# Kernel tuning notes

Hardware: AMD Instinct MI355X
Metric: run time of the kernel (lower is better)

The kernel has to match this reference:

```python
import jax, jax.numpy as jnp
import numpy as np

B, S, D_MODEL, H, NLAYERS, NHEADS = 16, 512, 768, 640, 2, 10
D_ATT = 2 * H  # 1280
HEAD_DIM = D_ATT // NHEADS  # 128


def _lstm_dir(xp, Whh, lengths, reverse):
    # xp: [B,S,4H] precomputed input projection (+bias); packed-sequence semantics:
    # state frozen and output zeroed for t >= length. torch gate order: i,f,g,o.
    Bs, Ss, H4 = xp.shape
    Hh = H4 // 4
    xpT = jnp.swapaxes(xp, 0, 1)  # [S,B,4H]
    ts = jnp.arange(Ss)
    if reverse:
        xpT = xpT[::-1]
        ts = ts[::-1]

    def step(carry, inp):
        h, c = carry
        x_t, t = inp
        g = x_t + h @ Whh.T
        i, f, gg, o = jnp.split(g, 4, axis=-1)
        i = jax.nn.sigmoid(i)
        f = jax.nn.sigmoid(f)
        gg = jnp.tanh(gg)
        o = jax.nn.sigmoid(o)
        c2 = f * c + i * gg
        h2 = o * jnp.tanh(c2)
        valid = (t < lengths)[:, None]
        h = jnp.where(valid, h2, h)
        c = jnp.where(valid, c2, c)
        return (h, c), jnp.where(valid, h, jnp.zeros_like(h))

    init = (jnp.zeros((Bs, Hh), xp.dtype), jnp.zeros((Bs, Hh), xp.dtype))
    _, ys = jax.lax.scan(step, init, (xpT, ts))
    if reverse:
        ys = ys[::-1]
    return jnp.swapaxes(ys, 0, 1)  # [B,S,H]


def _bilstm_layer(x, Wih, Whh, b, lengths):
    # Wih: [2,4H,in], Whh: [2,4H,H], b: [2,4H] (b_ih+b_hh combined)
    outs = []
    for d, rev in ((0, False), (1, True)):
        xp = jnp.einsum('bsi,gi->bsg', x, Wih[d]) + b[d]
        outs.append(_lstm_dir(xp, Whh[d], lengths, rev))
    return jnp.concatenate(outs, axis=-1)  # [B,S,2H]


def _forward(c_a_embeds, c_mask, c_lengths, Wih0, Whh0, b0, Wih1, Whh1, b1,
             Wq, bq, Wk, bk, Wv, bv):
    h = _bilstm_layer(c_a_embeds, Wih0, Whh0, b0, c_lengths)
    h = _bilstm_layer(h, Wih1, Whh1, b1, c_lengths)
    Bb, Ss, Dd = h.shape
    q = (h @ Wq.T + bq).reshape(Bb, Ss, NHEADS, HEAD_DIM)
    k = (h @ Wk.T + bk).reshape(Bb, Ss, NHEADS, HEAD_DIM)
    v = (h @ Wv.T + bv).reshape(Bb, Ss, NHEADS, HEAD_DIM)
    scores = jnp.einsum('bqhd,bkhd->bhqk', q, k) / np.float32(np.sqrt(HEAD_DIM))
    scores = scores + c_mask  # additive HF-style mask [B,1,1,S]
    probs = jax.nn.softmax(scores, axis=-1)
    ctx = jnp.einsum('bhqk,bkhd->bqhd', probs, v).reshape(Bb, Ss, Dd)
    return h + ctx


def setup_inputs() -> dict:
    key = jax.random.key(0)
    ks = jax.random.split(key, 20)
    c_a_embeds = jax.random.normal(ks[0], (B, S, D_MODEL), dtype=jnp.float32)
    c_lengths = jax.random.randint(ks[1], (B,), S // 2, S + 1, dtype=jnp.int32)
    valid = jnp.arange(S)[None, :] < c_lengths[:, None]
    c_mask = jnp.where(valid, 0.0, -10000.0).astype(jnp.float32)[:, None, None, :]
    sc = 1.0 / np.sqrt(H)

    def u(k, shape):
        return jax.random.uniform(k, shape, jnp.float32, -sc, sc)

    Wih0 = u(ks[2], (2, 4 * H, D_MODEL))
    Whh0 = u(ks[3], (2, 4 * H, H))
    b0 = u(ks[4], (2, 4 * H))
    Wih1 = u(ks[5], (2, 4 * H, 2 * H))
    Whh1 = u(ks[6], (2, 4 * H, H))
    b1 = u(ks[7], (2, 4 * H))
    sa = 1.0 / np.sqrt(D_ATT)
    Wq = jax.random.uniform(ks[8], (D_ATT, D_ATT), jnp.float32, -sa, sa)
    bq = jnp.zeros((D_ATT,), jnp.float32)
    Wk = jax.random.uniform(ks[9], (D_ATT, D_ATT), jnp.float32, -sa, sa)
    bk = jnp.zeros((D_ATT,), jnp.float32)
    Wv = jax.random.uniform(ks[10], (D_ATT, D_ATT), jnp.float32, -sa, sa)
    bv = jnp.zeros((D_ATT,), jnp.float32)
    return dict(c_a_embeds=c_a_embeds, c_mask=c_mask, c_lengths=c_lengths,
                Wih0=Wih0, Whh0=Whh0, b0=b0, Wih1=Wih1, Whh1=Whh1, b1=b1,
                Wq=Wq, bq=bq, Wk=Wk, bk=bk, Wv=Wv, bv=bv)


def reference(c_a_embeds, c_mask, c_lengths, Wih0, Whh0, b0, Wih1, Whh1, b1,
              Wq, bq, Wk, bk, Wv, bv):
    return _forward(c_a_embeds, c_mask, c_lengths, Wih0, Whh0, b0,
                    Wih1, Whh1, b1, Wq, bq, Wk, bk, Wv, bv)
```

## Files before the change

kernel.cpp:

```cpp
#include <hip/hip_runtime.h>

typedef __attribute__((ext_vector_type(8))) short short8;
typedef __attribute__((ext_vector_type(4))) float f32x4;
typedef __attribute__((ext_vector_type(4))) unsigned int u32x4;

#define MFMA(a,b,c) __builtin_amdgcn_mfma_f32_16x16x32_bf16((a),(b),(c),0,0,0)

#define B_  16
#define S_  512
#define DM_ 768
#define H_  640
#define G4_ 2560
#define DA_ 1280
#define NH_ 10
#define HD_ 128

static __device__ __forceinline__ unsigned short f2bf(float v) {
  unsigned u = __builtin_bit_cast(unsigned, v);
  u = (u + 0x7fffu + ((u >> 16) & 1u)) >> 16;
  return (unsigned short)u;
}
static __device__ __forceinline__ float bf2f(unsigned short u) {
  return __builtin_bit_cast(float, (unsigned)u << 16);
}
static __device__ __forceinline__ float sigm(float x) { return 1.0f / (1.0f + __expf(-x)); }
static __device__ __forceinline__ float tanh_c(float x) {
  x = fminf(fmaxf(x, -15.0f), 15.0f);
  float e = __expf(2.0f * x);
  return (e - 1.0f) / (e + 1.0f);
}

static __device__ __forceinline__ u32x4 load_coh16(const void* p) {
  u32x4 r;
  asm volatile("global_load_dwordx4 %0, %1, off sc0 sc1"
               : "=v"(r) : "v"(p) : "memory");
  return r;
}
static __device__ __forceinline__ void store_coh_u16(void* p, unsigned v) {
  asm volatile("global_store_short %0, %1, off sc0 sc1"
               :: "v"(p), "v"(v) : "memory");
}
static __device__ __forceinline__ void store_coh_u32(void* p, unsigned v) {
  asm volatile("global_store_dword %0, %1, off sc0 sc1"
               :: "v"(p), "v"(v) : "memory");
}
static __device__ __forceinline__ unsigned load_coh_u32(const void* p) {
  unsigned r;
  asm volatile("global_load_dword %0, %1, off sc0 sc1"
               : "=v"(r) : "v"(p) : "memory");
  return r;
}
#define WAIT_VM0() asm volatile("s_waitcnt vmcnt(0)" ::: "memory")

__global__ __launch_bounds__(256)
void cast_f32_bf16(const float* __restrict__ src, unsigned short* __restrict__ dst, int n4) {
  int i = blockIdx.x * 256 + threadIdx.x;
  if (i >= n4) return;
  float4 v = reinterpret_cast<const float4*>(src)[i];
  ushort4 o;
  o.x = f2bf(v.x); o.y = f2bf(v.y); o.z = f2bf(v.z); o.w = f2bf(v.w);
  reinterpret_cast<ushort4*>(dst)[i] = o;
}

__device__ __forceinline__ void gload_lds16(void* lds, const void* g) {
  __builtin_amdgcn_global_load_lds(
      (const __attribute__((address_space(1))) unsigned int*)g,
      (__attribute__((address_space(3))) unsigned int*)lds, 16, 0, 0);
}

template<int OUT_MODE>
__global__ __launch_bounds__(256)
void gemm_abt(const unsigned short* __restrict__ A, const unsigned short* __restrict__ W,
              const float* __restrict__ bias, void* __restrict__ Cout,
              int M, int N, int K) {
  __shared__ unsigned short lA[128 * 32];
  __shared__ unsigned short lB[128 * 32];
  const int tid = threadIdx.x;
  const int lane = tid & 63, wid = tid >> 6;
  const int nbn = N >> 7;
  const int mi = blockIdx.x / nbn, ni = blockIdx.x % nbn;
  const int l15 = lane & 15, lq = lane >> 4;

  f32x4 acc[4][4] = {};

  for (int k0 = 0; k0 < K; k0 += 32) {
#pragma unroll
    for (int part = 0; part < 2; ++part) {
      int linear = part * 256 + tid;
      int r = linear >> 2, cc = linear & 3;
      const unsigned short* ga = A + (size_t)(mi * 128 + r) * K + k0 + cc * 8;
      const unsigned short* gb = W + (size_t)(ni * 128 + r) * K + k0 + cc * 8;
      gload_lds16(&lA[(part * 256 + wid * 64) * 8], ga);
      gload_lds16(&lB[(part * 256 + wid * 64) * 8], gb);
    }
    __syncthreads();
    const int wm = (wid >> 1) * 64, wn = (wid & 1) * 64;
    short8 af[4], bfr[4];
#pragma unroll
    for (int m = 0; m < 4; ++m)
      af[m] = *(const short8*)&lA[(wm + m * 16 + l15) * 32 + lq * 8];
#pragma unroll
    for (int n = 0; n < 4; ++n)
      bfr[n] = *(const short8*)&lB[(wn + n * 16 + l15) * 32 + lq * 8];
#pragma unroll
    for (int m = 0; m < 4; ++m)
#pragma unroll
      for (int n = 0; n < 4; ++n)
        acc[m][n] = MFMA(af[m], bfr[n], acc[m][n]);
    __syncthreads();
  }

  const int wm = (wid >> 1) * 64, wn = (wid & 1) * 64;
#pragma unroll
  for (int n = 0; n < 4; ++n) {
    int col = ni * 128 + wn + n * 16 + l15;
    float bv = bias[col];
#pragma unroll
    for (int m = 0; m < 4; ++m) {
#pragma unroll
      for (int r = 0; r < 4; ++r) {
        int row = mi * 128 + wm + m * 16 + lq * 4 + r;
        float v = acc[m][n][r] + bv;
        if (OUT_MODE == 1) {
          ((unsigned short*)Cout)[(size_t)row * N + col] = f2bf(v);
        } else if (OUT_MODE == 2) {
          int bb = row >> 9, s = row & 511, hh = col >> 7, d = col & 127;
          ((unsigned short*)Cout)[(((size_t)(bb * NH_ + hh) * HD_ + d) << 9) + s] = f2bf(v);
        } else {
          int gate = col / 640, unit = col % 640;
          int slice = unit / 20, uu = unit % 20;
          int bb = row >> 9, tt = row & 511;
          size_t idx = (((size_t)slice * S_ + tt) * B_ + bb) * 80 + gate * 20 + uu;
          if (OUT_MODE == 3) ((float*)Cout)[idx] = v;
          else               ((unsigned short*)Cout)[idx] = f2bf(v);
        }
      }
    }
  }
}

template<bool XPF32>
__global__ __launch_bounds__(320)
void bilstm_layer(const void* __restrict__ xp_,
                  const unsigned short* __restrict__ whh_g,
                  const int* __restrict__ lengths,
                  unsigned short* __restrict__ h_ex,
                  int* __restrict__ flags, int flag_base,
                  unsigned short* __restrict__ out_bf)
{
  __shared__ unsigned short whh[80 * 648];
  __shared__ unsigned short hbuf[16 * 648];
  __shared__ float pre[16 * 80];
  __shared__ float xpbuf[16 * 80];
  __shared__ int len_s[16];

  const int tid = threadIdx.x;
  const int lane = tid & 63, wid = tid >> 6;
  const int wg = blockIdx.x;
  const int dir = wg >> 5, slice = wg & 31;
  const int J0 = slice * 20;
  const int l15 = lane & 15, lq = lane >> 4;

  for (int c = tid; c < 80 * 160; c += 320) {
    int r = c / 160, c4 = c % 160;
    int grow = (r / 20) * H_ + J0 + (r % 20);
    *(ushort4*)&whh[r * 648 + c4 * 4] =
        *(const ushort4*)&whh_g[((size_t)dir * G4_ + grow) * H_ + c4 * 4];
  }
  if (tid < 16) len_s[tid] = lengths[tid];
  __syncthreads();

  const int gb = tid / 20, gu = tid % 20;
  float c_st = 0.f, h_st = 0.f;

  const char* xps;
  if (XPF32)
    xps = (const char*)xp_ + ((size_t)dir * 32 + slice) * S_ * B_ * 80 * 4;
  else
    xps = (const char*)xp_ + ((size_t)dir * 32 + slice) * S_ * B_ * 80 * 2;

  float4  xv_f;
  ushort4 xv_h;
  {
    int t0 = dir ? (S_ - 1) : 0;
    if (XPF32) xv_f = *(const float4*)(xps + ((size_t)t0 * 1280 + tid * 4) * 4);
    else       xv_h = *(const ushort4*)(xps + ((size_t)t0 * 1280 + tid * 4) * 2);
  }

  for (int s = 0; s < S_; ++s) {
    const int t = dir ? (S_ - 1 - s) : s;
    float4  xn_f;
    ushort4 xn_h;
    {
      int tn = dir ? (S_ - 2 - s) : (s + 1);
      tn = tn < 0 ? 0 : (tn > S_ - 1 ? S_ - 1 : tn);
      if (XPF32) xn_f = *(const float4*)(xps + ((size_t)tn * 1280 + tid * 4) * 4);
      else       xn_h = *(const ushort4*)(xps + ((size_t)tn * 1280 + tid * 4) * 2);
    }

    {
      const unsigned short* src = h_ex + (size_t)(dir * 2 + (s & 1)) * B_ * H_;
      u32x4 hv[4];
      int bs[4], os[4];
#pragma unroll
      for (int j = 0; j < 4; ++j) {
        int c = tid + j * 320;
        bs[j] = c / 80; os[j] = c % 80;
        hv[j] = load_coh16(src + (size_t)bs[j] * 640 + os[j] * 8);
      }
      WAIT_VM0();
      __builtin_amdgcn_sched_barrier(0);
#pragma unroll
      for (int j = 0; j < 4; ++j)
        *(u32x4*)&hbuf[bs[j] * 648 + os[j] * 8] = hv[j];
    }
    if (XPF32) {
      *(float4*)&xpbuf[tid * 4] = xv_f;
    } else {
      *(ushort4*)&((unsigned short*)xpbuf)[tid * 4] = xv_h;
    }
    __syncthreads();

    f32x4 acc0 = {0.f, 0.f, 0.f, 0.f}, acc1 = {0.f, 0.f, 0.f, 0.f};
#pragma unroll
    for (int kk = 0; kk < 20; kk += 2) {
      short8 a0 = *(const short8*)&hbuf[l15 * 648 + kk * 32 + lq * 8];
      short8 b0v = *(const short8*)&whh[(wid * 16 + l15) * 648 + kk * 32 + lq * 8];
      acc0 = MFMA(a0, b0v, acc0);
      short8 a1 = *(const short8*)&hbuf[l15 * 648 + (kk + 1) * 32 + lq * 8];
      short8 b1v = *(const short8*)&whh[(wid * 16 + l15) * 648 + (kk + 1) * 32 + lq * 8];
      acc1 = MFMA(a1, b1v, acc1);
    }
#pragma unroll
    for (int r = 0; r < 4; ++r)
      pre[(lq * 4 + r) * 80 + wid * 16 + l15] = acc0[r] + acc1[r];
    __syncthreads();

    {
      float xi, xf, xg, xo;
      if (XPF32) {
        xi = xpbuf[gb * 80 + gu];
        xf = xpbuf[gb * 80 + 20 + gu];
        xg = xpbuf[gb * 80 + 40 + gu];
        xo = xpbuf[gb * 80 + 60 + gu];
      } else {
        const unsigned short* xb = (const unsigned short*)xpbuf;
        xi = bf2f(xb[gb * 80 + gu]);
        xf = bf2f(xb[gb * 80 + 20 + gu]);
        xg = bf2f(xb[gb * 80 + 40 + gu]);
        xo = bf2f(xb[gb * 80 + 60 + gu]);
      }
      float gi = pre[gb * 80 + gu]      + xi;
      float gf = pre[gb * 80 + 20 + gu] + xf;
      float gg = pre[gb * 80 + 40 + gu] + xg;
      float go = pre[gb * 80 + 60 + gu] + xo;
      float i_ = sigm(gi), f_ = sigm(gf);
      float g_ = tanh_c(gg), o_ = sigm(go);
      float c2 = f_ * c_st + i_ * g_;
      float h2 = o_ * tanh_c(c2);
      bool valid = t < len_s[gb];
      c_st = valid ? c2 : c_st;
      h_st = valid ? h2 : h_st;
      unsigned hb = f2bf(h_st);
      store_coh_u16(h_ex + (size_t)(dir * 2 + ((s + 1) & 1)) * B_ * H_
                         + (size_t)gb * H_ + J0 + gu, hb);
      float yv = valid ? h_st : 0.f;
      out_bf[((size_t)(gb * S_ + t)) * DA_ + dir * H_ + J0 + gu] = f2bf(yv);
    }

    WAIT_VM0();
    __syncthreads();
    const int target = flag_base + s + 1;
    if (tid == 0)
      store_coh_u32(flags + (size_t)wg * 32, (unsigned)target);
    if (wid == 0) {
      const int* fp = flags + (size_t)(dir * 32 + (lane & 31)) * 32;
      for (;;) {
        unsigned v = load_coh_u32(fp);
        WAIT_VM0();
        if (__all((int)v >= target)) break;
      }
    }
    __syncthreads();
    xv_f = xn_f; xv_h = xn_h;
  }
}

__global__ __launch_bounds__(256)
void attn_fused(const unsigned short* __restrict__ q, const unsigned short* __restrict__ k,
                const unsigned short* __restrict__ vT, const float* __restrict__ mask,
                const unsigned short* __restrict__ h1, float* __restrict__ out)
{
  __shared__ unsigned short p_lds[64 * 512];
  const int tid = threadIdx.x, lane = tid & 63, wid = tid >> 6;
  const int bx = blockIdx.x;
  const int b = bx / 80, rem = bx % 80, h = rem / 8, qt = rem % 8;
  const int l15 = lane & 15, lq = lane >> 4;
  const int qrow0 = qt * 64 + wid * 16;

  short8 qf[4];
  {
    const unsigned short* qb = q + ((size_t)(b * S_ + qrow0 + l15)) * DA_ + h * HD_ + lq * 8;
#pragma unroll
    for (int ks = 0; ks < 4; ++ks) qf[ks] = *(const short8*)(qb + ks * 32);
  }
  f32x4 sc[32];
#pragma unroll
  for (int nt = 0; nt < 32; ++nt) {
    f32x4 a = {0.f, 0.f, 0.f, 0.f};
    const unsigned short* kb = k + ((size_t)(b * S_ + nt * 16 + l15)) * DA_ + h * HD_ + lq * 8;
#pragma unroll
    for (int ks = 0; ks < 4; ++ks) {
      short8 bf = *(const short8*)(kb + ks * 32);
      a = MFMA(qf[ks], bf, a);
    }
    sc[nt] = a;
  }
  const float scl = 0.08838834764831845f;
  float mx[4] = {-1e30f, -1e30f, -1e30f, -1e30f};
#pragma unroll
  for (int nt = 0; nt < 32; ++nt) {
    float mv = mask[b * S_ + nt * 16 + l15];
#pragma unroll
    for (int r = 0; r < 4; ++r) {
      float v = sc[nt][r] * scl + mv;
      sc[nt][r] = v;
      mx[r] = fmaxf(mx[r], v);
    }
  }
#pragma unroll
  for (int r = 0; r < 4; ++r) {
    mx[r] = fmaxf(mx[r], __shfl_xor(mx[r], 1));
    mx[r] = fmaxf(mx[r], __shfl_xor(mx[r], 2));
    mx[r] = fmaxf(mx[r], __shfl_xor(mx[r], 4));
    mx[r] = fmaxf(mx[r], __shfl_xor(mx[r], 8));
  }
  float sm[4] = {0.f, 0.f, 0.f, 0.f};
#pragma unroll
  for (int nt = 0; nt < 32; ++nt)
#pragma unroll
    for (int r = 0; r < 4; ++r) {
      float p = __expf(sc[nt][r] - mx[r]);
      sc[nt][r] = p; sm[r] += p;
    }
#pragma unroll
  for (int r = 0; r < 4; ++r) {
    sm[r] += __shfl_xor(sm[r], 1);
    sm[r] += __shfl_xor(sm[r], 2);
    sm[r] += __shfl_xor(sm[r], 4);
    sm[r] += __shfl_xor(sm[r], 8);
    sm[r] = 1.0f / sm[r];
  }
#pragma unroll
  for (int nt = 0; nt < 32; ++nt)
#pragma unroll
    for (int r = 0; r < 4; ++r) {
      int row = wid * 16 + lq * 4 + r;
      int byte = row * 1024 + (nt * 16 + l15) * 2;
      byte ^= (row & 7) << 4;
      *(unsigned short*)((char*)p_lds + byte) = f2bf(sc[nt][r] * sm[r]);
    }
  __syncthreads();

  f32x4 oa[8] = {};
#pragma unroll
  for (int kk = 0; kk < 16; ++kk) {
    int row = wid * 16 + l15;
    int byte = row * 1024 + (kk * 32 + lq * 8) * 2;
    byte ^= (row & 7) << 4;
    short8 pa = *(const short8*)((char*)p_lds + byte);
    const unsigned short* vb = vT + ((size_t)(b * NH_ + h) * HD_ + l15) * S_ + kk * 32 + lq * 8;
#pragma unroll
    for (int n = 0; n < 8; ++n) {
      short8 bv = *(const short8*)(vb + n * 16 * S_);
      oa[n] = MFMA(pa, bv, oa[n]);
    }
  }
#pragma unroll
  for (int n = 0; n < 8; ++n)
#pragma unroll
    for (int r = 0; r < 4; ++r) {
      int row = qrow0 + lq * 4 + r;
      int col = h * HD_ + n * 16 + l15;
      size_t idx = ((size_t)(b * S_ + row)) * DA_ + col;
      out[idx] = bf2f(h1[idx]) + oa[n][r];
    }
}

extern "C" void kernel_launch(void* const* d_in, const int* in_sizes, int n_in,
                              void* d_out, int out_size, void* d_ws, size_t ws_size,
                              hipStream_t stream) {
  const float* x    = (const float*)d_in[0];
  const float* mask = (const float*)d_in[1];
  const int*   lens = (const int*)d_in[2];
  const float* Wih0 = (const float*)d_in[3];
  const float* Whh0 = (const float*)d_in[4];
  const float* b0   = (const float*)d_in[5];
  const float* Wih1 = (const float*)d_in[6];
  const float* Whh1 = (const float*)d_in[7];
  const float* b1   = (const float*)d_in[8];
  const float* Wq   = (const float*)d_in[9];
  const float* bq   = (const float*)d_in[10];
  const float* Wk   = (const float*)d_in[11];
  const float* bk   = (const float*)d_in[12];
  const float* Wv   = (const float*)d_in[13];
  const float* bv   = (const float*)d_in[14];

  const size_t SZ_wb_ih1 = (size_t)2 * G4_ * DA_ * 2;
  const size_t SZ_wb_hh  = (size_t)2 * G4_ * H_ * 2;
  const size_t SZ_wb_qkv = (size_t)DA_ * DA_ * 2;
  const size_t SZ_tok_bf = (size_t)B_ * S_ * DA_ * 2;
  const size_t SZ_h_ex   = (size_t)2 * 2 * B_ * H_ * 2;
  const size_t SZ_flags  = (size_t)64 * 32 * 4;
  const size_t SZ_xbf    = (size_t)B_ * S_ * DM_ * 2;
  const size_t SZ_wb_ih0 = (size_t)2 * G4_ * DM_ * 2;
  const size_t SZ_regA   = SZ_xbf + SZ_wb_ih0 + SZ_wb_hh;
  const size_t SZ_xp_f32 = (size_t)2 * B_ * S_ * G4_ * 4;
  const size_t SZ_xp_bf  = SZ_xp_f32 / 2;

  const size_t persist = SZ_wb_ih1 + SZ_wb_hh + 3 * SZ_wb_qkv + 2 * SZ_tok_bf
                       + SZ_h_ex + SZ_flags;
  const size_t need_A = persist + SZ_regA + SZ_xp_f32;
  const bool xpf32 = (ws_size >= need_A + 4096);

  char* ws = (char*)d_ws;
  size_t off = 0;
  auto alloc = [&](size_t bytes) { char* p = ws + off; off += bytes; return p; };

  unsigned short* wb_ih1 = (unsigned short*)alloc(SZ_wb_ih1);
  unsigned short* wb_hh1 = (unsigned short*)alloc(SZ_wb_hh);
  unsigned short* wb_q   = (unsigned short*)alloc(SZ_wb_qkv);
  unsigned short* wb_k   = (unsigned short*)alloc(SZ_wb_qkv);
  unsigned short* wb_v   = (unsigned short*)alloc(SZ_wb_qkv);
  unsigned short* h0bf   = (unsigned short*)alloc(SZ_tok_bf);
  unsigned short* h1bf   = (unsigned short*)alloc(SZ_tok_bf);
  unsigned short* h_ex   = (unsigned short*)alloc(SZ_h_ex);
  int*            flags  = (int*)alloc(SZ_flags);

  char* regA = alloc(SZ_regA);
  unsigned short* xbf    = (unsigned short*)regA;
  unsigned short* wb_ih0 = (unsigned short*)(regA + SZ_xbf);
  unsigned short* wb_hh0 = (unsigned short*)(regA + SZ_xbf + SZ_wb_ih0);
  unsigned short* qbf    = (unsigned short*)regA;

  char* regB = alloc(xpf32 ? SZ_xp_f32 : SZ_xp_bf);
  void*           xp     = (void*)regB;
  unsigned short* kbf    = (unsigned short*)regB;
  unsigned short* vtbf   = (unsigned short*)(regB + SZ_tok_bf);

  hipMemsetAsync(h_ex, 0, SZ_h_ex + SZ_flags, stream);

  auto cast = [&](const float* s, unsigned short* d, size_t n) {
    int n4 = (int)(n / 4);
    cast_f32_bf16<<<(n4 + 255) / 256, 256, 0, stream>>>(s, d, n4);
  };
  cast(Wih0, wb_ih0, (size_t)2 * G4_ * DM_);
  cast(Whh0, wb_hh0, (size_t)2 * G4_ * H_);
  cast(Wih1, wb_ih1, (size_t)2 * G4_ * DA_);
  cast(Whh1, wb_hh1, (size_t)2 * G4_ * H_);
  cast(Wq, wb_q, (size_t)DA_ * DA_);
  cast(Wk, wb_k, (size_t)DA_ * DA_);
  cast(Wv, wb_v, (size_t)DA_ * DA_);
  cast(x, xbf, (size_t)B_ * S_ * DM_);

  const int M = B_ * S_;
  const size_t xp_dir_elems = (size_t)32 * S_ * B_ * 80;

  if (xpf32) {
    gemm_abt<3><<<(M / 128) * (G4_ / 128), 256, 0, stream>>>(
        xbf, wb_ih0, b0, xp, M, G4_, DM_);
    gemm_abt<3><<<(M / 128) * (G4_ / 128), 256, 0, stream>>>(
        xbf, wb_ih0 + (size_t)G4_ * DM_, b0 + G4_,
        (float*)xp + xp_dir_elems, M, G4_, DM_);
    bilstm_layer<true><<<64, 320, 0, stream>>>(xp, wb_hh0, lens, h_ex, flags, 0, h0bf);
  } else {
    gemm_abt<4><<<(M / 128) * (G4_ / 128), 256, 0, stream>>>(
        xbf, wb_ih0, b0, xp, M, G4_, DM_);
    gemm_abt<4><<<(M / 128) * (G4_ / 128), 256, 0, stream>>>(
        xbf, wb_ih0 + (size_t)G4_ * DM_, b0 + G4_,
        (unsigned short*)xp + xp_dir_elems, M, G4_, DM_);
    bilstm_layer<false><<<64, 320, 0, stream>>>(xp, wb_hh0, lens, h_ex, flags, 0, h0bf);
  }

  if (xpf32) {
    gemm_abt<3><<<(M / 128) * (G4_ / 128), 256, 0, stream>>>(
        h0bf, wb_ih1, b1, xp, M, G4_, DA_);
    gemm_abt<3><<<(M / 128) * (G4_ / 128), 256, 0, stream>>>(
        h0bf, wb_ih1 + (size_t)G4_ * DA_, b1 + G4_,
        (float*)xp + xp_dir_elems, M, G4_, DA_);
  } else {
    gemm_abt<4><<<(M / 128) * (G4_ / 128), 256, 0, stream>>>(
        h0bf, wb_ih1, b1, xp, M, G4_, DA_);
    gemm_abt<4><<<(M / 128) * (G4_ / 128), 256, 0, stream>>>(
        h0bf, wb_ih1 + (size_t)G4_ * DA_, b1 + G4_,
        (unsigned short*)xp + xp_dir_elems, M, G4_, DA_);
  }
  hipMemsetAsync(h_ex, 0, SZ_h_ex, stream);
  if (xpf32)
    bilstm_layer<true><<<64, 320, 0, stream>>>(xp, wb_hh1, lens, h_ex, flags, S_, h1bf);
  else
    bilstm_layer<false><<<64, 320, 0, stream>>>(xp, wb_hh1, lens, h_ex, flags, S_, h1bf);

  gemm_abt<1><<<(M / 128) * (DA_ / 128), 256, 0, stream>>>(
      h1bf, wb_q, bq, qbf, M, DA_, DA_);
  gemm_abt<1><<<(M / 128) * (DA_ / 128), 256, 0, stream>>>(
      h1bf, wb_k, bk, kbf, M, DA_, DA_);
  gemm_abt<2><<<(M / 128) * (DA_ / 128), 256, 0, stream>>>(
      h1bf, wb_v, bv, vtbf, M, DA_, DA_);
  attn_fused<<<B_ * NH_ * 8, 256, 0, stream>>>(qbf, kbf, vtbf, mask, h1bf,
                                               (float*)d_out);
}
```

Before: 4.132 ms.

## Replace flag barrier with step-tagged hidden-state packets in BiLSTM recurrence

The per-step cross-workgroup synchronisation in the recurrent kernel drops its separate flag array and spin barrier. Each workgroup now packs three bf16 hidden values plus a 16-bit step tag into 64-bit coherent stores, and consumers spin directly on the data until every tag reaches the current step. This removes one global round trip (flag store, then flag poll, then data load) per timestep. The cost is more scattered LDS writes when unpacking and reliance on 64-bit store atomicity, with double buffering keeping it correct.

```diff
diff --git a/kernel.cpp b/kernel.cpp
--- a/kernel.cpp
+++ b/kernel.cpp
@@ -2,7 +2,6 @@
 
 typedef __attribute__((ext_vector_type(8))) short short8;
 typedef __attribute__((ext_vector_type(4))) float f32x4;
-typedef __attribute__((ext_vector_type(4))) unsigned int u32x4;
 
 #define MFMA(a,b,c) __builtin_amdgcn_mfma_f32_16x16x32_bf16((a),(b),(c),0,0,0)
 
@@ -30,25 +29,15 @@
   return (e - 1.0f) / (e + 1.0f);
 }
 
-static __device__ __forceinline__ u32x4 load_coh16(const void* p) {
-  u32x4 r;
-  asm volatile("global_load_dwordx4 %0, %1, off sc0 sc1"
+static __device__ __forceinline__ unsigned long long load_coh64(const void* p) {
+  unsigned long long r;
+  asm volatile("global_load_dwordx2 %0, %1, off sc0 sc1"
                : "=v"(r) : "v"(p) : "memory");
   return r;
 }
-static __device__ __forceinline__ void store_coh_u16(void* p, unsigned v) {
-  asm volatile("global_store_short %0, %1, off sc0 sc1"
+static __device__ __forceinline__ void store_coh64(void* p, unsigned long long v) {
+  asm volatile("global_store_dwordx2 %0, %1, off sc0 sc1"
                :: "v"(p), "v"(v) : "memory");
-}
-static __device__ __forceinline__ void store_coh_u32(void* p, unsigned v) {
-  asm volatile("global_store_dword %0, %1, off sc0 sc1"
-               :: "v"(p), "v"(v) : "memory");
-}
-static __device__ __forceinline__ unsigned load_coh_u32(const void* p) {
-  unsigned r;
-  asm volatile("global_load_dword %0, %1, off sc0 sc1"
-               : "=v"(r) : "v"(p) : "memory");
-  return r;
 }
 #define WAIT_VM0() asm volatile("s_waitcnt vmcnt(0)" ::: "memory")
 
@@ -139,19 +128,22 @@
   }
 }
 
+#define NQ_  110
+#define SLAB_ 896
+
 template<bool XPF32>
 __global__ __launch_bounds__(320)
 void bilstm_layer(const void* __restrict__ xp_,
                   const unsigned short* __restrict__ whh_g,
                   const int* __restrict__ lengths,
-                  unsigned short* __restrict__ h_ex,
-                  int* __restrict__ flags, int flag_base,
+                  char* __restrict__ h_ex2,
                   unsigned short* __restrict__ out_bf)
 {
   __shared__ unsigned short whh[80 * 648];
   __shared__ unsigned short hbuf[16 * 648];
   __shared__ float pre[16 * 80];
   __shared__ float xpbuf[16 * 80];
+  __shared__ unsigned short staged[336];
   __shared__ int len_s[16];
 
   const int tid = threadIdx.x;
@@ -172,6 +164,15 @@
 
   const int gb = tid / 20, gu = tid % 20;
   float c_st = 0.f, h_st = 0.f;
+
+  const int cp  = tid / 10;
+  const int qi0 = (tid % 10) * 11;
+  const char* csrc[2];
+  csrc[0] = h_ex2 + ((size_t)(dir * 2 + 0) * 32 + cp) * SLAB_ + (size_t)qi0 * 8;
+  csrc[1] = h_ex2 + ((size_t)(dir * 2 + 1) * 32 + cp) * SLAB_ + (size_t)qi0 * 8;
+  char* pdst[2];
+  pdst[0] = h_ex2 + ((size_t)(dir * 2 + 0) * 32 + slice) * SLAB_;
+  pdst[1] = h_ex2 + ((size_t)(dir * 2 + 1) * 32 + slice) * SLAB_;
 
   const char* xps;
   if (XPF32)
@@ -198,21 +199,29 @@
       else       xn_h = *(const ushort4*)(xps + ((size_t)tn * 1280 + tid * 4) * 2);
     }
 
+    unsigned long long qv[11];
     {
-      const unsigned short* src = h_ex + (size_t)(dir * 2 + (s & 1)) * B_ * H_;
-      u32x4 hv[4];
-      int bs[4], os[4];
-#pragma unroll
-      for (int j = 0; j < 4; ++j) {
-        int c = tid + j * 320;
-        bs[j] = c / 80; os[j] = c % 80;
-        hv[j] = load_coh16(src + (size_t)bs[j] * 640 + os[j] * 8);
+      const char* sb = csrc[s & 1];
+      for (;;) {
+#pragma unroll
+        for (int j = 0; j < 11; ++j) qv[j] = load_coh64(sb + j * 8);
+        WAIT_VM0();
+        __builtin_amdgcn_sched_barrier(0);
+        bool ok = true;
+#pragma unroll
+        for (int j = 0; j < 11; ++j) ok &= ((int)(qv[j] >> 48) >= s);
+        if (__all(ok)) break;
       }
-      WAIT_VM0();
-      __builtin_amdgcn_sched_barrier(0);
-#pragma unroll
-      for (int j = 0; j < 4; ++j)
-        *(u32x4*)&hbuf[bs[j] * 648 + os[j] * 8] = hv[j];
+#pragma unroll
+      for (int j = 0; j < 11; ++j) {
+        int off0 = (qi0 + j) * 3;
+        unsigned short v0 = (unsigned short)(qv[j]);
+        unsigned short v1 = (unsigned short)(qv[j] >> 16);
+        unsigned short v2 = (unsigned short)(qv[j] >> 32);
+        if (off0 < 320)     hbuf[(off0 / 20) * 648 + cp * 20 + (off0 % 20)] = v0;
+        if (off0 + 1 < 320) hbuf[((off0 + 1) / 20) * 648 + cp * 20 + ((off0 + 1) % 20)] = v1;
+        if (off0 + 2 < 320) hbuf[((off0 + 2) / 20) * 648 + cp * 20 + ((off0 + 2) % 20)] = v2;
+      }
     }
     if (XPF32) {
       *(float4*)&xpbuf[tid * 4] = xv_f;
@@ -261,27 +270,23 @@
       bool valid = t < len_s[gb];
       c_st = valid ? c2 : c_st;
       h_st = valid ? h2 : h_st;
-      unsigned hb = f2bf(h_st);
-      store_coh_u16(h_ex + (size_t)(dir * 2 + ((s + 1) & 1)) * B_ * H_
-                         + (size_t)gb * H_ + J0 + gu, hb);
+      staged[gb * 20 + gu] = f2bf(h_st);
+    }
+    __syncthreads();
+
+    if (tid < NQ_) {
+      unsigned long long q =
+            (unsigned long long)staged[tid * 3]
+          | ((unsigned long long)staged[tid * 3 + 1] << 16)
+          | ((unsigned long long)staged[tid * 3 + 2] << 32)
+          | ((unsigned long long)(unsigned)(s + 1) << 48);
+      store_coh64(pdst[(s + 1) & 1] + (size_t)tid * 8, q);
+    }
+    {
+      bool valid = t < len_s[gb];
       float yv = valid ? h_st : 0.f;
       out_bf[((size_t)(gb * S_ + t)) * DA_ + dir * H_ + J0 + gu] = f2bf(yv);
     }
-
-    WAIT_VM0();
-    __syncthreads();
-    const int target = flag_base + s + 1;
-    if (tid == 0)
-      store_coh_u32(flags + (size_t)wg * 32, (unsigned)target);
-    if (wid == 0) {
-      const int* fp = flags + (size_t)(dir * 32 + (lane & 31)) * 32;
-      for (;;) {
-        unsigned v = load_coh_u32(fp);
-        WAIT_VM0();
-        if (__all((int)v >= target)) break;
-      }
-    }
-    __syncthreads();
     xv_f = xn_f; xv_h = xn_h;
   }
 }
@@ -410,8 +415,7 @@
   const size_t SZ_wb_hh  = (size_t)2 * G4_ * H_ * 2;
   const size_t SZ_wb_qkv = (size_t)DA_ * DA_ * 2;
   const size_t SZ_tok_bf = (size_t)B_ * S_ * DA_ * 2;
-  const size_t SZ_h_ex   = (size_t)2 * 2 * B_ * H_ * 2;
-  const size_t SZ_flags  = (size_t)64 * 32 * 4;
+  const size_t SZ_h_ex2  = (size_t)2 * 2 * 32 * SLAB_;
   const size_t SZ_xbf    = (size_t)B_ * S_ * DM_ * 2;
   const size_t SZ_wb_ih0 = (size_t)2 * G4_ * DM_ * 2;
   const size_t SZ_regA   = SZ_xbf + SZ_wb_ih0 + SZ_wb_hh;
@@ -419,7 +423,7 @@
   const size_t SZ_xp_bf  = SZ_xp_f32 / 2;
 
   const size_t persist = SZ_wb_ih1 + SZ_wb_hh + 3 * SZ_wb_qkv + 2 * SZ_tok_bf
-                       + SZ_h_ex + SZ_flags;
+                       + SZ_h_ex2;
   const size_t need_A = persist + SZ_regA + SZ_xp_f32;
   const bool xpf32 = (ws_size >= need_A + 4096);
 
@@ -434,8 +438,7 @@
   unsigned short* wb_v   = (unsigned short*)alloc(SZ_wb_qkv);
   unsigned short* h0bf   = (unsigned short*)alloc(SZ_tok_bf);
   unsigned short* h1bf   = (unsigned short*)alloc(SZ_tok_bf);
-  unsigned short* h_ex   = (unsigned short*)alloc(SZ_h_ex);
-  int*            flags  = (int*)alloc(SZ_flags);
+  char*           h_ex2  = alloc(SZ_h_ex2);
 
   char* regA = alloc(SZ_regA);
   unsigned short* xbf    = (unsigned short*)regA;
@@ -448,7 +451,7 @@
   unsigned short* kbf    = (unsigned short*)regB;
   unsigned short* vtbf   = (unsigned short*)(regB + SZ_tok_bf);
 
-  hipMemsetAsync(h_ex, 0, SZ_h_ex + SZ_flags, stream);
+  hipMemsetAsync(h_ex2, 0, SZ_h_ex2, stream);
 
   auto cast = [&](const float* s, unsigned short* d, size_t n) {
     int n4 = (int)(n / 4);
@@ -472,14 +475,14 @@
     gemm_abt<3><<<(M / 128) * (G4_ / 128), 256, 0, stream>>>(
         xbf, wb_ih0 + (size_t)G4_ * DM_, b0 + G4_,
         (float*)xp + xp_dir_elems, M, G4_, DM_);
-    bilstm_layer<true><<<64, 320, 0, stream>>>(xp, wb_hh0, lens, h_ex, flags, 0, h0bf);
+    bilstm_layer<true><<<64, 320, 0, stream>>>(xp, wb_hh0, lens, h_ex2, h0bf);
   } else {
     gemm_abt<4><<<(M / 128) * (G4_ / 128), 256, 0, stream>>>(
         xbf, wb_ih0, b0, xp, M, G4_, DM_);
     gemm_abt<4><<<(M / 128) * (G4_ / 128), 256, 0, stream>>>(
         xbf, wb_ih0 + (size_t)G4_ * DM_, b0 + G4_,
         (unsigned short*)xp + xp_dir_elems, M, G4_, DM_);
-    bilstm_layer<false><<<64, 320, 0, stream>>>(xp, wb_hh0, lens, h_ex, flags, 0, h0bf);
+    bilstm_layer<false><<<64, 320, 0, stream>>>(xp, wb_hh0, lens, h_ex2, h0bf);
   }
 
   if (xpf32) {
@@ -495,11 +498,11 @@
         h0bf, wb_ih1 + (size_t)G4_ * DA_, b1 + G4_,
         (unsigned short*)xp + xp_dir_elems, M, G4_, DA_);
   }
-  hipMemsetAsync(h_ex, 0, SZ_h_ex, stream);
+  hipMemsetAsync(h_ex2, 0, SZ_h_ex2, stream);
   if (xpf32)
-    bilstm_layer<true><<<64, 320, 0, stream>>>(xp, wb_hh1, lens, h_ex, flags, S_, h1bf);
+    bilstm_layer<true><<<64, 320, 0, stream>>>(xp, wb_hh1, lens, h_ex2, h1bf);
   else
-    bilstm_layer<false><<<64, 320, 0, stream>>>(xp, wb_hh1, lens, h_ex, flags, S_, h1bf);
+    bilstm_layer<false><<<64, 320, 0, stream>>>(xp, wb_hh1, lens, h_ex2, h1bf);
 
   gemm_abt<1><<<(M / 128) * (DA_ / 128), 256, 0, stream>>>(
       h1bf, wb_q, bq, qbf, M, DA_, DA_);
```

New measurement: 4.748 ms. +14.9%, slower.

## Restructure BiLSTM recurrence: register-resident Whh, in-wave gate shuffles, slab-based partial sync

Applied to the files above, without the earlier changes.

The persistent BiLSTM kernel now runs 16 workgroups of 640 threads per direction instead of 32 of 320, each handling 40 hidden units. The recurrent weights are held in registers rather than LDS, and the xp layout is interleaved so that each lane's MFMA output maps to one gate. Gates are combined with lane shuffles, which removes the pre/xpbuf LDS round-trip and a barrier. The global all-to-all exchange is replaced with per-slice 1280-byte slabs: one wave publishes its slab and flag, while eight waves each poll two producers' flags and pull their slabs into LDS. This is meant to cut per-step latency and barrier count, at the cost of heavy register pressure (20 short8 B fragments per lane) and a more intricate sync protocol.

```diff
diff --git a/kernel.cpp b/kernel.cpp
--- a/kernel.cpp
+++ b/kernel.cpp
@@ -14,6 +14,9 @@
 #define DA_ 1280
 #define NH_ 10
 #define HD_ 128
+#define U_   40
+#define NWG_ 16
+#define SLABB_ 1280
 
 static __device__ __forceinline__ unsigned short f2bf(float v) {
   unsigned u = __builtin_bit_cast(unsigned, v);
@@ -36,17 +39,17 @@
                : "=v"(r) : "v"(p) : "memory");
   return r;
 }
-static __device__ __forceinline__ void store_coh_u16(void* p, unsigned v) {
-  asm volatile("global_store_short %0, %1, off sc0 sc1"
+static __device__ __forceinline__ void store_coh16(void* p, u32x4 v) {
+  asm volatile("global_store_dwordx4 %0, %1, off sc0 sc1"
                :: "v"(p), "v"(v) : "memory");
 }
 static __device__ __forceinline__ void store_coh_u32(void* p, unsigned v) {
   asm volatile("global_store_dword %0, %1, off sc0 sc1"
                :: "v"(p), "v"(v) : "memory");
 }
-static __device__ __forceinline__ unsigned load_coh_u32(const void* p) {
+static __device__ __forceinline__ unsigned poll_u32(const void* p) {
   unsigned r;
-  asm volatile("global_load_dword %0, %1, off sc0 sc1"
+  asm volatile("global_load_dword %0, %1, off sc0 sc1\n\ts_waitcnt vmcnt(0)"
                : "=v"(r) : "v"(p) : "memory");
   return r;
 }
@@ -127,10 +130,10 @@
           int bb = row >> 9, s = row & 511, hh = col >> 7, d = col & 127;
           ((unsigned short*)Cout)[(((size_t)(bb * NH_ + hh) * HD_ + d) << 9) + s] = f2bf(v);
         } else {
-          int gate = col / 640, unit = col % 640;
-          int slice = unit / 20, uu = unit % 20;
+          int gate = col / 640, un = col % 640;
+          int sl = un / U_, uu = un % U_;
           int bb = row >> 9, tt = row & 511;
-          size_t idx = (((size_t)slice * S_ + tt) * B_ + bb) * 80 + gate * 20 + uu;
+          size_t idx = ((((size_t)sl * S_ + tt) * 4 + gate) * U_ + uu) * 16 + bb;
           if (OUT_MODE == 3) ((float*)Cout)[idx] = v;
           else               ((unsigned short*)Cout)[idx] = f2bf(v);
         }
@@ -140,149 +143,143 @@
 }
 
 template<bool XPF32>
-__global__ __launch_bounds__(320)
+__global__ __launch_bounds__(640)
 void bilstm_layer(const void* __restrict__ xp_,
                   const unsigned short* __restrict__ whh_g,
                   const int* __restrict__ lengths,
-                  unsigned short* __restrict__ h_ex,
-                  int* __restrict__ flags, int flag_base,
+                  char* __restrict__ h_ex2,
+                  int* __restrict__ flags,
                   unsigned short* __restrict__ out_bf)
 {
-  __shared__ unsigned short whh[80 * 648];
   __shared__ unsigned short hbuf[16 * 648];
-  __shared__ float pre[16 * 80];
-  __shared__ float xpbuf[16 * 80];
+  __shared__ unsigned short staged[16 * U_];
   __shared__ int len_s[16];
 
   const int tid = threadIdx.x;
-  const int lane = tid & 63, wid = tid >> 6;
+  const int lane = tid & 63, w = tid >> 6;
   const int wg = blockIdx.x;
-  const int dir = wg >> 5, slice = wg & 31;
-  const int J0 = slice * 20;
+  const int dir = wg >> 4, slice = wg & 15;
+  const int J0 = slice * U_;
   const int l15 = lane & 15, lq = lane >> 4;
-
-  for (int c = tid; c < 80 * 160; c += 320) {
-    int r = c / 160, c4 = c % 160;
-    int grow = (r / 20) * H_ + J0 + (r % 20);
-    *(ushort4*)&whh[r * 648 + c4 * 4] =
-        *(const ushort4*)&whh_g[((size_t)dir * G4_ + grow) * H_ + c4 * 4];
+  const int uloc = 4 * w + (l15 >> 2);
+  const int gate = l15 & 3;
+
+  short8 bfr[20];
+  {
+    const unsigned short* wrow =
+        whh_g + ((size_t)dir * G4_ + gate * H_ + J0 + uloc) * H_ + lq * 8;
+#pragma unroll
+    for (int kk = 0; kk < 20; ++kk) bfr[kk] = *(const short8*)(wrow + kk * 32);
   }
   if (tid < 16) len_s[tid] = lengths[tid];
+  for (int c = tid; c < 16 * 648; c += 640) hbuf[c] = 0;
   __syncthreads();
 
-  const int gb = tid / 20, gu = tid % 20;
-  float c_st = 0.f, h_st = 0.f;
-
-  const char* xps;
-  if (XPF32)
-    xps = (const char*)xp_ + ((size_t)dir * 32 + slice) * S_ * B_ * 80 * 4;
-  else
-    xps = (const char*)xp_ + ((size_t)dir * 32 + slice) * S_ * B_ * 80 * 2;
-
-  float4  xv_f;
-  ushort4 xv_h;
+  float cst[4] = {0.f, 0.f, 0.f, 0.f};
+  float hst[4] = {0.f, 0.f, 0.f, 0.f};
+
+  const char* xps = (const char*)xp_ +
+      ((size_t)dir * NWG_ + slice) * S_ * (4 * U_ * 16) * (XPF32 ? 4 : 2);
+  const int xoff_e = (gate * U_ + uloc) * 16 + lq * 4;
+
+  float4  xvf; ushort4 xvh;
   {
     int t0 = dir ? (S_ - 1) : 0;
-    if (XPF32) xv_f = *(const float4*)(xps + ((size_t)t0 * 1280 + tid * 4) * 4);
-    else       xv_h = *(const ushort4*)(xps + ((size_t)t0 * 1280 + tid * 4) * 2);
+    if (XPF32) xvf = *(const float4*)(xps + ((size_t)t0 * (4*U_*16) + xoff_e) * 4);
+    else       xvh = *(const ushort4*)(xps + ((size_t)t0 * (4*U_*16) + xoff_e) * 2);
   }
 
   for (int s = 0; s < S_; ++s) {
     const int t = dir ? (S_ - 1 - s) : s;
-    float4  xn_f;
-    ushort4 xn_h;
+
+    f32x4 a0 = {0.f,0.f,0.f,0.f}, a1 = {0.f,0.f,0.f,0.f};
+#pragma unroll
+    for (int kk = 0; kk < 20; kk += 2) {
+      short8 av0 = *(const short8*)&hbuf[l15 * 648 + kk * 32 + lq * 8];
+      a0 = MFMA(av0, bfr[kk], a0);
+      short8 av1 = *(const short8*)&hbuf[l15 * 648 + (kk + 1) * 32 + lq * 8];
+      a1 = MFMA(av1, bfr[kk + 1], a1);
+    }
+
+    float yv[4];
+#pragma unroll
+    for (int r = 0; r < 4; ++r) {
+      float xq = XPF32 ? ((const float*)&xvf)[r] : bf2f(((const unsigned short*)&xvh)[r]);
+      float pre = a0[r] + a1[r] + xq;
+      float x1 = __shfl_xor(pre, 1);
+      float x2 = __shfl_xor(pre, 2);
+      float x3 = __shfl_xor(pre, 3);
+      float ip = gate == 0 ? pre : gate == 1 ? x1 : gate == 2 ? x2 : x3;
+      float fp = gate == 0 ? x1 : gate == 1 ? pre : gate == 2 ? x3 : x2;
+      float gp = gate == 0 ? x2 : gate == 1 ? x3 : gate == 2 ? pre : x1;
+      float op = gate == 0 ? x3 : gate == 1 ? x2 : gate == 2 ? x1 : pre;
+      float i_ = sigm(ip), f_ = sigm(fp);
+      float g_ = tanh_c(gp), o_ = sigm(op);
+      float c2 = f_ * cst[r] + i_ * g_;
+      float h2 = o_ * tanh_c(c2);
+      int b = lq * 4 + r;
+      bool valid = t < len_s[b];
+      cst[r] = valid ? c2 : cst[r];
+      hst[r] = valid ? h2 : hst[r];
+      yv[r] = valid ? hst[r] : 0.f;
+      if (gate == 0) staged[b * U_ + uloc] = f2bf(hst[r]);
+    }
+    __syncthreads();
+
+    if (s + 1 < S_) {
+      const int tgt = s + 1;
+      char* par_base = h_ex2 + (size_t)((dir * 2 + ((s + 1) & 1)) * NWG_) * SLABB_;
+      if (w == 8) {
+        u32x4 d0 = *(const u32x4*)&staged[lane * 8];
+        u32x4 d1 = *(const u32x4*)&staged[(64 + (lane & 15)) * 8];
+        char* myslab = par_base + (size_t)slice * SLABB_;
+        store_coh16(myslab + lane * 16, d0);
+        if (lane < 16) store_coh16(myslab + (64 + lane) * 16, d1);
+        WAIT_VM0();
+        if (lane == 0)
+          store_coh_u32(flags + (size_t)(dir * NWG_ + slice) * 32, (unsigned)tgt);
+      } else if (w < 8) {
+        const int pA = 2 * w, pB = 2 * w + 1;
+        const int* fp = flags + (size_t)(dir * NWG_ + (lane < 32 ? pA : pB)) * 32;
+        for (;;) {
+          unsigned v = poll_u32(fp);
+          if (__all((int)v >= tgt)) break;
+        }
+        const char* sA = par_base + (size_t)pA * SLABB_;
+        const char* sB = par_base + (size_t)pB * SLABB_;
+        u32x4 qA0 = load_coh16(sA + lane * 16);
+        u32x4 qA1 = load_coh16(sA + (64 + (lane & 15)) * 16);
+        u32x4 qB0 = load_coh16(sB + lane * 16);
+        u32x4 qB1 = load_coh16(sB + (64 + (lane & 15)) * 16);
+        WAIT_VM0();
+        __builtin_amdgcn_sched_barrier(0);
+        {
+          int c = lane, b = c / 5, m = c - 5 * b;
+          *(u32x4*)&hbuf[b * 648 + pA * U_ + m * 8] = qA0;
+          *(u32x4*)&hbuf[b * 648 + pB * U_ + m * 8] = qB0;
+        }
+        if (lane < 16) {
+          int c = 64 + lane, b = c / 5, m = c - 5 * b;
+          *(u32x4*)&hbuf[b * 648 + pA * U_ + m * 8] = qA1;
+          *(u32x4*)&hbuf[b * 648 + pB * U_ + m * 8] = qB1;
+        }
+      }
+    }
+
+    if (gate == 0) {
+#pragma unroll
+      for (int r = 0; r < 4; ++r) {
+        int b = lq * 4 + r;
+        out_bf[((size_t)(b * S_ + t)) * DA_ + dir * H_ + J0 + uloc] = f2bf(yv[r]);
+      }
+    }
     {
       int tn = dir ? (S_ - 2 - s) : (s + 1);
       tn = tn < 0 ? 0 : (tn > S_ - 1 ? S_ - 1 : tn);
-      if (XPF32) xn_f = *(const float4*)(xps + ((size_t)tn * 1280 + tid * 4) * 4);
-      else       xn_h = *(const ushort4*)(xps + ((size_t)tn * 1280 + tid * 4) * 2);
-    }
-
-    {
-      const unsigned short* src = h_ex + (size_t)(dir * 2 + (s & 1)) * B_ * H_;
-      u32x4 hv[4];
-      int bs[4], os[4];
-#pragma unroll
-      for (int j = 0; j < 4; ++j) {
-        int c = tid + j * 320;
-        bs[j] = c / 80; os[j] = c % 80;
-        hv[j] = load_coh16(src + (size_t)bs[j] * 640 + os[j] * 8);
-      }
-      WAIT_VM0();
-      __builtin_amdgcn_sched_barrier(0);
-#pragma unroll
-      for (int j = 0; j < 4; ++j)
-        *(u32x4*)&hbuf[bs[j] * 648 + os[j] * 8] = hv[j];
-    }
-    if (XPF32) {
-      *(float4*)&xpbuf[tid * 4] = xv_f;
-    } else {
-      *(ushort4*)&((unsigned short*)xpbuf)[tid * 4] = xv_h;
+      if (XPF32) xvf = *(const float4*)(xps + ((size_t)tn * (4*U_*16) + xoff_e) * 4);
+      else       xvh = *(const ushort4*)(xps + ((size_t)tn * (4*U_*16) + xoff_e) * 2);
     }
     __syncthreads();
-
-    f32x4 acc0 = {0.f, 0.f, 0.f, 0.f}, acc1 = {0.f, 0.f, 0.f, 0.f};
-#pragma unroll
-    for (int kk = 0; kk < 20; kk += 2) {
-      short8 a0 = *(const short8*)&hbuf[l15 * 648 + kk * 32 + lq * 8];
-      short8 b0v = *(const short8*)&whh[(wid * 16 + l15) * 648 + kk * 32 + lq * 8];
-      acc0 = MFMA(a0, b0v, acc0);
-      short8 a1 = *(const short8*)&hbuf[l15 * 648 + (kk + 1) * 32 + lq * 8];
-      short8 b1v = *(const short8*)&whh[(wid * 16 + l15) * 648 + (kk + 1) * 32 + lq * 8];
-      acc1 = MFMA(a1, b1v, acc1);
-    }
-#pragma unroll
-    for (int r = 0; r < 4; ++r)
-      pre[(lq * 4 + r) * 80 + wid * 16 + l15] = acc0[r] + acc1[r];
-    __syncthreads();
-
-    {
-      float xi, xf, xg, xo;
-      if (XPF32) {
-        xi = xpbuf[gb * 80 + gu];
-        xf = xpbuf[gb * 80 + 20 + gu];
-        xg = xpbuf[gb * 80 + 40 + gu];
-        xo = xpbuf[gb * 80 + 60 + gu];
-      } else {
-        const unsigned short* xb = (const unsigned short*)xpbuf;
-        xi = bf2f(xb[gb * 80 + gu]);
-        xf = bf2f(xb[gb * 80 + 20 + gu]);
-        xg = bf2f(xb[gb * 80 + 40 + gu]);
-        xo = bf2f(xb[gb * 80 + 60 + gu]);
-      }
-      float gi = pre[gb * 80 + gu]      + xi;
-      float gf = pre[gb * 80 + 20 + gu] + xf;
-      float gg = pre[gb * 80 + 40 + gu] + xg;
-      float go = pre[gb * 80 + 60 + gu] + xo;
-      float i_ = sigm(gi), f_ = sigm(gf);
-      float g_ = tanh_c(gg), o_ = sigm(go);
-      float c2 = f_ * c_st + i_ * g_;
-      float h2 = o_ * tanh_c(c2);
-      bool valid = t < len_s[gb];
-      c_st = valid ? c2 : c_st;
-      h_st = valid ? h2 : h_st;
-      unsigned hb = f2bf(h_st);
-      store_coh_u16(h_ex + (size_t)(dir * 2 + ((s + 1) & 1)) * B_ * H_
-                         + (size_t)gb * H_ + J0 + gu, hb);
-      float yv = valid ? h_st : 0.f;
-      out_bf[((size_t)(gb * S_ + t)) * DA_ + dir * H_ + J0 + gu] = f2bf(yv);
-    }
-
-    WAIT_VM0();
-    __syncthreads();
-    const int target = flag_base + s + 1;
-    if (tid == 0)
-      store_coh_u32(flags + (size_t)wg * 32, (unsigned)target);
-    if (wid == 0) {
-      const int* fp = flags + (size_t)(dir * 32 + (lane & 31)) * 32;
-      for (;;) {
-        unsigned v = load_coh_u32(fp);
-        WAIT_VM0();
-        if (__all((int)v >= target)) break;
-      }
-    }
-    __syncthreads();
-    xv_f = xn_f; xv_h = xn_h;
   }
 }
 
@@ -410,8 +407,8 @@
   const size_t SZ_wb_hh  = (size_t)2 * G4_ * H_ * 2;
   const size_t SZ_wb_qkv = (size_t)DA_ * DA_ * 2;
   const size_t SZ_tok_bf = (size_t)B_ * S_ * DA_ * 2;
-  const size_t SZ_h_ex   = (size_t)2 * 2 * B_ * H_ * 2;
-  const size_t SZ_flags  = (size_t)64 * 32 * 4;
+  const size_t SZ_h_ex2  = (size_t)2 * 2 * NWG_ * SLABB_;
+  const size_t SZ_flags  = (size_t)2 * NWG_ * 32 * 4;
   const size_t SZ_xbf    = (size_t)B_ * S_ * DM_ * 2;
   const size_t SZ_wb_ih0 = (size_t)2 * G4_ * DM_ * 2;
   const size_t SZ_regA   = SZ_xbf + SZ_wb_ih0 + SZ_wb_hh;
@@ -419,7 +416,7 @@
   const size_t SZ_xp_bf  = SZ_xp_f32 / 2;
 
   const size_t persist = SZ_wb_ih1 + SZ_wb_hh + 3 * SZ_wb_qkv + 2 * SZ_tok_bf
-                       + SZ_h_ex + SZ_flags;
+                       + SZ_h_ex2 + SZ_flags;
   const size_t need_A = persist + SZ_regA + SZ_xp_f32;
   const bool xpf32 = (ws_size >= need_A + 4096);
 
@@ -434,7 +431,7 @@
   unsigned short* wb_v   = (unsigned short*)alloc(SZ_wb_qkv);
   unsigned short* h0bf   = (unsigned short*)alloc(SZ_tok_bf);
   unsigned short* h1bf   = (unsigned short*)alloc(SZ_tok_bf);
-  unsigned short* h_ex   = (unsigned short*)alloc(SZ_h_ex);
+  char*           h_ex2  = alloc(SZ_h_ex2);
   int*            flags  = (int*)alloc(SZ_flags);
 
   char* regA = alloc(SZ_regA);
@@ -448,7 +445,7 @@
   unsigned short* kbf    = (unsigned short*)regB;
   unsigned short* vtbf   = (unsigned short*)(regB + SZ_tok_bf);
 
-  hipMemsetAsync(h_ex, 0, SZ_h_ex + SZ_flags, stream);
+  hipMemsetAsync(h_ex2, 0, SZ_h_ex2 + SZ_flags, stream);
 
   auto cast = [&](const float* s, unsigned short* d, size_t n) {
     int n4 = (int)(n / 4);
@@ -464,7 +461,7 @@
   cast(x, xbf, (size_t)B_ * S_ * DM_);
 
   const int M = B_ * S_;
-  const size_t xp_dir_elems = (size_t)32 * S_ * B_ * 80;
+  const size_t xp_dir_elems = (size_t)NWG_ * S_ * 4 * U_ * 16;
 
   if (xpf32) {
     gemm_abt<3><<<(M / 128) * (G4_ / 128), 256, 0, stream>>>(
@@ -472,14 +469,14 @@
     gemm_abt<3><<<(M / 128) * (G4_ / 128), 256, 0, stream>>>(
         xbf, wb_ih0 + (size_t)G4_ * DM_, b0 + G4_,
         (float*)xp + xp_dir_elems, M, G4_, DM_);
-    bilstm_layer<true><<<64, 320, 0, stream>>>(xp, wb_hh0, lens, h_ex, flags, 0, h0bf);
+    bilstm_layer<true><<<32, 640, 0, stream>>>(xp, wb_hh0, lens, h_ex2, flags, h0bf);
   } else {
     gemm_abt<4><<<(M / 128) * (G4_ / 128), 256, 0, stream>>>(
         xbf, wb_ih0, b0, xp, M, G4_, DM_);
     gemm_abt<4><<<(M / 128) * (G4_ / 128), 256, 0, stream>>>(
         xbf, wb_ih0 + (size_t)G4_ * DM_, b0 + G4_,
         (unsigned short*)xp + xp_dir_elems, M, G4_, DM_);
-    bilstm_layer<false><<<64, 320, 0, stream>>>(xp, wb_hh0, lens, h_ex, flags, 0, h0bf);
+    bilstm_layer<false><<<32, 640, 0, stream>>>(xp, wb_hh0, lens, h_ex2, flags, h0bf);
   }
 
   if (xpf32) {
@@ -495,11 +492,11 @@
         h0bf, wb_ih1 + (size_t)G4_ * DA_, b1 + G4_,
         (unsigned short*)xp + xp_dir_elems, M, G4_, DA_);
   }
-  hipMemsetAsync(h_ex, 0, SZ_h_ex, stream);
+  hipMemsetAsync(h_ex2, 0, SZ_h_ex2 + SZ_flags, stream);
   if (xpf32)
-    bilstm_layer<true><<<64, 320, 0, stream>>>(xp, wb_hh1, lens, h_ex, flags, S_, h1bf);
+    bilstm_layer<true><<<32, 640, 0, stream>>>(xp, wb_hh1, lens, h_ex2, flags, h1bf);
   else
-    bilstm_layer<false><<<64, 320, 0, stream>>>(xp, wb_hh1, lens, h_ex, flags, S_, h1bf);
+    bilstm_layer<false><<<32, 640, 0, stream>>>(xp, wb_hh1, lens, h_ex2, flags, h1bf);
 
   gemm_abt<1><<<(M / 128) * (DA_ / 128), 256, 0, stream>>>(
       h1bf, wb_q, bq, qbf, M, DA_, DA_);
```

New measurement: 6.077 ms. 1.47x slower.
